# Kernel optimization log

Measured on AMD Instinct MI355X. Metric: run time of the kernel, lower is better.

Reference implementation:

```python
import jax, jax.numpy as jnp
import numpy as np

N_NODES = 500000   # embedding table / pi rows
K = 32             # mixture components (communities)
D = 64             # embedding dim
B = 65536          # batch of node ids


def setup_inputs() -> dict:
    key = jax.random.key(0)
    k1, k2, k3, k4, k5 = jax.random.split(key, 5)
    embedding = jax.random.normal(k1, (N_NODES, D), dtype=jnp.float32)
    centroid = jax.random.normal(k2, (K, D), dtype=jnp.float32)
    # SPD covariance per component: A A^T * s + I
    A = jax.random.normal(k3, (K, D, D), dtype=jnp.float32) * 0.1
    cov = jnp.einsum('kde,kfe->kdf', A, A) + jnp.eye(D, dtype=jnp.float32)[None]
    # responsibilities (rows sum to 1, like predict_proba output)
    pi = jax.nn.softmax(jax.random.normal(k4, (N_NODES, K), dtype=jnp.float32), axis=-1)
    input_labels = jax.random.randint(k5, (B,), 0, N_NODES)
    return {
        'embedding': embedding,
        'centroid': centroid,
        'cov': cov,
        'pi': pi,
        'input_labels': input_labels,
    }


def reference(embedding, centroid, cov, pi, input_labels):
    # x = node_embedding(input_labels): (B, D)
    x = embedding[input_labels]
    inv_cov = jnp.linalg.inv(cov)                 # (K, D, D)
    _, logdet = jnp.linalg.slogdet(cov)           # (K,)
    diff = x[:, None, :] - centroid[None, :, :]   # (B, K, D)
    # batched Mahalanobis distance per component: (B, K)
    quad = jnp.einsum('bkd,kde,bke->bk', diff, inv_cov, diff)
    log2pi = jnp.log(jnp.asarray(2.0 * np.pi, dtype=x.dtype))
    logpdf = -0.5 * (D * log2pi + logdet[None, :] + quad)  # (B, K)
    resp = pi[input_labels]                       # (B, K)
    # original: ret_loss = abs(sum_i sum_k pi[i,k] * logpdf[i,k])
    return jnp.abs(jnp.sum(resp * logpdf))
```

## Files before the change

kernel.cpp:

```cpp
#include <hip/hip_runtime.h>

#define LOG2PI 1.8378770664093453f
#define LN2    0.6931471805599453f

typedef short short8 __attribute__((ext_vector_type(8)));
typedef float f32x4 __attribute__((ext_vector_type(4)));

__device__ __forceinline__ unsigned short f2bf(float f) {
    unsigned int u = __builtin_bit_cast(unsigned int, f);
    u = (u + 0x7FFFu + ((u >> 16) & 1u)) >> 16;
    return (unsigned short)u;
}
__device__ __forceinline__ float bf2f(unsigned short h) {
    unsigned int u = ((unsigned int)h) << 16;
    return __builtin_bit_cast(float, u);
}
__device__ __forceinline__ short8 pack8(float4 f0, float4 f1) {
    short8 r;
    r[0] = (short)f2bf(f0.x); r[1] = (short)f2bf(f0.y);
    r[2] = (short)f2bf(f0.z); r[3] = (short)f2bf(f0.w);
    r[4] = (short)f2bf(f1.x); r[5] = (short)f2bf(f1.y);
    r[6] = (short)f2bf(f1.z); r[7] = (short)f2bf(f1.w);
    return r;
}
__device__ __forceinline__ float rdlane(float v, int lane) {
    return __builtin_bit_cast(float, __builtin_amdgcn_readlane(__builtin_bit_cast(int, v), lane));
}

__global__ __launch_bounds__(512) void prep_kernel(
    const float* __restrict__ cov, const float* __restrict__ centroid,
    unsigned short* __restrict__ wW, float* __restrict__ wV2,
    float* __restrict__ wC, float* __restrict__ wAcc)
{
    __shared__ float rowbuf[2][64];
    __shared__ float Mi[64 * 65];
    const int k = blockIdx.x;
    const int tid = threadIdx.x;
    const int w = tid >> 6;
    const int l = tid & 63;

    float a[8];
#pragma unroll
    for (int r = 0; r < 8; ++r)
        a[r] = cov[(size_t)k * 4096 + (w * 8 + r) * 64 + l];

    if (k == 0 && tid == 0) wAcc[0] = 0.0f;

    float ld2 = 0.0f;
    for (int phase = 0; phase < 8; ++phase) {
        const bool owner = (w == phase);
#pragma unroll
        for (int jr = 0; jr < 8; ++jr) {
            const int j = phase * 8 + jr;
            if (owner) rowbuf[jr & 1][l] = a[jr];
            __syncthreads();
            float prow = rowbuf[jr & 1][l];
            float p = rdlane(prow, j);
            float pinv = __builtin_amdgcn_rcpf(p);
            ld2 += __log2f(p);
            float rjs = prow * pinv;
            float rjsp = (l == j) ? 1.0f + pinv : rjs;
#pragma unroll
            for (int r = 0; r < 8; ++r) {
                float cji = rdlane(a[r], j);
                a[r] = fmaf(-cji, rjsp, a[r]);
            }
            if (owner) a[jr] = (l == j) ? pinv : rjs;
        }
    }

#pragma unroll
    for (int r = 0; r < 8; ++r) Mi[(w * 8 + r) * 65 + l] = a[r];
    __syncthreads();

    if (tid < 64) {
        const int t = tid;
        float cme = centroid[k * 64 + t];
        float y = 0.0f;
#pragma unroll
        for (int e = 0; e < 64; ++e)
            y = fmaf(Mi[t * 65 + e], rdlane(cme, e), y);
        wV2[k * 64 + t] = 2.0f * y;
        float cy = cme * y;
#pragma unroll
        for (int off = 32; off > 0; off >>= 1) cy += __shfl_down(cy, off);
        if (t == 0) wC[k] = 64.0f * LOG2PI + ld2 * LN2 + cy;
    }

    {
        const int m = l & 15, qd = l >> 4;
        const int ntl = tid >> 7, s2 = (tid >> 6) & 1;
        const int d = ntl * 16 + m;
        const int e0 = s2 * 32 + qd * 8;
        float4 f0, f1;
        f0.x = Mi[d * 65 + e0 + 0]; f0.y = Mi[d * 65 + e0 + 1];
        f0.z = Mi[d * 65 + e0 + 2]; f0.w = Mi[d * 65 + e0 + 3];
        f1.x = Mi[d * 65 + e0 + 4]; f1.y = Mi[d * 65 + e0 + 5];
        f1.z = Mi[d * 65 + e0 + 6]; f1.w = Mi[d * 65 + e0 + 7];
        short8 pk = pack8(f0, f1);
        ((uint4*)wW)[((k * 4 + ntl) * 2 + s2) * 64 + l] = __builtin_bit_cast(uint4, pk);
    }
}

__global__ __launch_bounds__(256) void main_kernel(
    const float* __restrict__ emb, const float* __restrict__ pi,
    const int* __restrict__ labels, const unsigned short* __restrict__ wW,
    const float* __restrict__ wV2, const float* __restrict__ wC,
    float* __restrict__ wAcc)
{
    __shared__ int lab[128];
    __shared__ unsigned short Xs[128 * 72];
    __shared__ float Rg[128 * 36];
    __shared__ float vq[2048];
    __shared__ float cdet[32];
    __shared__ float red[4];

    const int tid = threadIdx.x;
    const int row0 = blockIdx.x * 128;

    if (tid < 128) lab[tid] = labels[row0 + tid];
    if (tid < 32) cdet[tid] = wC[tid];
    {
        const float4* v4 = (const float4*)wV2;
        *(float4*)&vq[tid * 8]     = v4[tid * 2];
        *(float4*)&vq[tid * 8 + 4] = v4[tid * 2 + 1];
    }
    __syncthreads();

    {
        int r = tid >> 1, h = tid & 1;
        const float4* e4 = (const float4*)(emb + (size_t)lab[r] * 64 + h * 32);
#pragma unroll
        for (int q = 0; q < 4; ++q) {
            float4 f0 = e4[q * 2], f1 = e4[q * 2 + 1];
            short8 pk = pack8(f0, f1);
            *(short8*)&Xs[r * 72 + h * 32 + q * 8] = pk;
        }
    }
    {
        const float4* pi4 = (const float4*)pi;
#pragma unroll
        for (int it = 0; it < 4; ++it) {
            int id = it * 256 + tid;
            int r = id >> 3, c = id & 7;
            float4 f = pi4[(size_t)lab[r] * 8 + c];
            *(float4*)&Rg[r * 36 + c * 4] = f;
        }
    }
    __syncthreads();

    const int w = tid >> 6, l = tid & 63;
    const int m = l & 15, qd = l >> 4;

    short8 afr[8][2];
#pragma unroll
    for (int rt = 0; rt < 8; ++rt) {
        int row = rt * 16 + m;
#pragma unroll
        for (int s = 0; s < 2; ++s)
            afr[rt][s] = *(const short8*)&Xs[row * 72 + s * 32 + qd * 8];
    }

    float qa[8][4] = {};
    float part = 0.0f;
    const uint4* wf4 = (const uint4*)wW;

    for (int nt = 0; nt < 32; ++nt) {
        int gnt = w * 32 + nt;
        uint4 u0 = wf4[(gnt * 2 + 0) * 64 + l];
        uint4 u1 = wf4[(gnt * 2 + 1) * 64 + l];
        short8 b0 = __builtin_bit_cast(short8, u0);
        short8 b1 = __builtin_bit_cast(short8, u1);
        float vv = vq[gnt * 16 + m];
        int dcol = (nt & 3) * 16 + m;
#pragma unroll
        for (int rt = 0; rt < 8; ++rt) {
            f32x4 cc = {0.0f, 0.0f, 0.0f, 0.0f};
            cc = __builtin_amdgcn_mfma_f32_16x16x32_bf16(afr[rt][0], b0, cc, 0, 0, 0);
            cc = __builtin_amdgcn_mfma_f32_16x16x32_bf16(afr[rt][1], b1, cc, 0, 0, 0);
#pragma unroll
            for (int r2 = 0; r2 < 4; ++r2) {
                int rowl = rt * 16 + qd * 4 + r2;
                float xv = bf2f(Xs[rowl * 72 + dcol]);
                qa[rt][r2] = fmaf(xv, cc[r2] - vv, qa[rt][r2]);
            }
        }
        if ((nt & 3) == 3) {
            int kk = w * 8 + (nt >> 2);
            float cd = cdet[kk] * 0.0625f;
#pragma unroll
            for (int rt = 0; rt < 8; ++rt) {
#pragma unroll
                for (int r2 = 0; r2 < 4; ++r2) {
                    int rowl = rt * 16 + qd * 4 + r2;
                    part = fmaf(Rg[rowl * 36 + kk], qa[rt][r2] + cd, part);
                    qa[rt][r2] = 0.0f;
                }
            }
        }
    }

    for (int off = 32; off > 0; off >>= 1) part += __shfl_down(part, off);
    if (l == 0) red[w] = part;
    __syncthreads();
    if (tid == 0) atomicAdd(wAcc, red[0] + red[1] + red[2] + red[3]);
}

__global__ void fin_kernel(const float* __restrict__ wAcc, float* __restrict__ out) {
    out[0] = fabsf(0.5f * wAcc[0]);
}

extern "C" void kernel_launch(void* const* d_in, const int* in_sizes, int n_in,
                              void* d_out, int out_size, void* d_ws, size_t ws_size,
                              hipStream_t stream) {
    const float* emb    = (const float*)d_in[0];
    const float* cent   = (const float*)d_in[1];
    const float* cov    = (const float*)d_in[2];
    const float* pi     = (const float*)d_in[3];
    const int*   labels = (const int*)d_in[4];
    float* out = (float*)d_out;

    char* w = (char*)d_ws;
    unsigned short* wW = (unsigned short*)w;
    float* wV2 = (float*)(w + 262144);
    float* wC  = (float*)(w + 270336);
    float* wAcc = (float*)(w + 270464);

    prep_kernel<<<32, 512, 0, stream>>>(cov, cent, wW, wV2, wC, wAcc);
    main_kernel<<<512, 256, 0, stream>>>(emb, pi, labels, wW, wV2, wC, wAcc);
    fin_kernel<<<1, 1, 0, stream>>>(wAcc, out);
}
```

Measured before the change: 247.6 us.

## Permute bf16 K-dim layout to keep x values in registers, fuse final reduction

Permutes the bf16 packing order of embedding rows and inverse-covariance fragments so that each lane's x values for the Mahalanobis weighting land in two packed registers. These are loaded once instead of being read from LDS inside the MFMA loop. The component loop is restructured into explicit per-component blocks with the four column tiles unrolled. The separate finalize kernel is removed in favour of a last-block-done atomic counter, which saves a launch at the cost of more register pressure and extra atomics.

```diff
diff --git a/kernel.cpp b/kernel.cpp
--- a/kernel.cpp
+++ b/kernel.cpp
@@ -11,18 +11,6 @@
     u = (u + 0x7FFFu + ((u >> 16) & 1u)) >> 16;
     return (unsigned short)u;
 }
-__device__ __forceinline__ float bf2f(unsigned short h) {
-    unsigned int u = ((unsigned int)h) << 16;
-    return __builtin_bit_cast(float, u);
-}
-__device__ __forceinline__ short8 pack8(float4 f0, float4 f1) {
-    short8 r;
-    r[0] = (short)f2bf(f0.x); r[1] = (short)f2bf(f0.y);
-    r[2] = (short)f2bf(f0.z); r[3] = (short)f2bf(f0.w);
-    r[4] = (short)f2bf(f1.x); r[5] = (short)f2bf(f1.y);
-    r[6] = (short)f2bf(f1.z); r[7] = (short)f2bf(f1.w);
-    return r;
-}
 __device__ __forceinline__ float rdlane(float v, int lane) {
     return __builtin_bit_cast(float, __builtin_amdgcn_readlane(__builtin_bit_cast(int, v), lane));
 }
@@ -30,7 +18,7 @@
 __global__ __launch_bounds__(512) void prep_kernel(
     const float* __restrict__ cov, const float* __restrict__ centroid,
     unsigned short* __restrict__ wW, float* __restrict__ wV2,
-    float* __restrict__ wC, float* __restrict__ wAcc)
+    float* __restrict__ wC, float* __restrict__ wAcc, unsigned int* __restrict__ wCnt)
 {
     __shared__ float rowbuf[2][64];
     __shared__ float Mi[64 * 65];
@@ -44,7 +32,7 @@
     for (int r = 0; r < 8; ++r)
         a[r] = cov[(size_t)k * 4096 + (w * 8 + r) * 64 + l];
 
-    if (k == 0 && tid == 0) wAcc[0] = 0.0f;
+    if (k == 0 && tid == 0) { wAcc[0] = 0.0f; wCnt[0] = 0u; }
 
     float ld2 = 0.0f;
     for (int phase = 0; phase < 8; ++phase) {
@@ -91,13 +79,12 @@
         const int m = l & 15, qd = l >> 4;
         const int ntl = tid >> 7, s2 = (tid >> 6) & 1;
         const int d = ntl * 16 + m;
-        const int e0 = s2 * 32 + qd * 8;
-        float4 f0, f1;
-        f0.x = Mi[d * 65 + e0 + 0]; f0.y = Mi[d * 65 + e0 + 1];
-        f0.z = Mi[d * 65 + e0 + 2]; f0.w = Mi[d * 65 + e0 + 3];
-        f1.x = Mi[d * 65 + e0 + 4]; f1.y = Mi[d * 65 + e0 + 5];
-        f1.z = Mi[d * 65 + e0 + 6]; f1.w = Mi[d * 65 + e0 + 7];
-        short8 pk = pack8(f0, f1);
+        const int base = s2 * 8 + qd * 2;
+        const float* Mr = &Mi[d * 65];
+        short8 pk;
+#pragma unroll
+        for (int i = 0; i < 8; ++i)
+            pk[i] = (short)f2bf(Mr[(i & 3) * 16 + base + (i >> 2)]);
         ((uint4*)wW)[((k * 4 + ntl) * 2 + s2) * 64 + l] = __builtin_bit_cast(uint4, pk);
     }
 }
@@ -106,7 +93,8 @@
     const float* __restrict__ emb, const float* __restrict__ pi,
     const int* __restrict__ labels, const unsigned short* __restrict__ wW,
     const float* __restrict__ wV2, const float* __restrict__ wC,
-    float* __restrict__ wAcc)
+    float* __restrict__ wAcc, unsigned int* __restrict__ wCnt,
+    float* __restrict__ out)
 {
     __shared__ int lab[128];
     __shared__ unsigned short Xs[128 * 72];
@@ -129,12 +117,22 @@
 
     {
         int r = tid >> 1, h = tid & 1;
-        const float4* e4 = (const float4*)(emb + (size_t)lab[r] * 64 + h * 32);
-#pragma unroll
-        for (int q = 0; q < 4; ++q) {
-            float4 f0 = e4[q * 2], f1 = e4[q * 2 + 1];
-            short8 pk = pack8(f0, f1);
-            *(short8*)&Xs[r * 72 + h * 32 + q * 8] = pk;
+        const float* erow = emb + (size_t)lab[r] * 64 + h * 8;
+        float xv[4][8];
+#pragma unroll
+        for (int c16 = 0; c16 < 4; ++c16) {
+            float4 f0 = *(const float4*)(erow + c16 * 16);
+            float4 f1 = *(const float4*)(erow + c16 * 16 + 4);
+            xv[c16][0] = f0.x; xv[c16][1] = f0.y; xv[c16][2] = f0.z; xv[c16][3] = f0.w;
+            xv[c16][4] = f1.x; xv[c16][5] = f1.y; xv[c16][6] = f1.z; xv[c16][7] = f1.w;
+        }
+#pragma unroll
+        for (int g = 0; g < 4; ++g) {
+            short8 pk;
+#pragma unroll
+            for (int idx = 0; idx < 8; ++idx)
+                pk[idx] = (short)f2bf(xv[idx & 3][g * 2 + (idx >> 2)]);
+            *(short8*)&Xs[r * 72 + h * 32 + g * 8] = pk;
         }
     }
     {
@@ -160,54 +158,71 @@
         for (int s = 0; s < 2; ++s)
             afr[rt][s] = *(const short8*)&Xs[row * 72 + s * 32 + qd * 8];
     }
-
-    float qa[8][4] = {};
+    uint2 xr[8][4];
+#pragma unroll
+    for (int rt = 0; rt < 8; ++rt)
+#pragma unroll
+        for (int r2 = 0; r2 < 4; ++r2) {
+            int rowl = rt * 16 + qd * 4 + r2;
+            xr[rt][r2] = *(const uint2*)&Xs[rowl * 72 + m * 4];
+        }
+
     float part = 0.0f;
     const uint4* wf4 = (const uint4*)wW;
 
-    for (int nt = 0; nt < 32; ++nt) {
-        int gnt = w * 32 + nt;
-        uint4 u0 = wf4[(gnt * 2 + 0) * 64 + l];
-        uint4 u1 = wf4[(gnt * 2 + 1) * 64 + l];
-        short8 b0 = __builtin_bit_cast(short8, u0);
-        short8 b1 = __builtin_bit_cast(short8, u1);
-        float vv = vq[gnt * 16 + m];
-        int dcol = (nt & 3) * 16 + m;
-#pragma unroll
-        for (int rt = 0; rt < 8; ++rt) {
-            f32x4 cc = {0.0f, 0.0f, 0.0f, 0.0f};
-            cc = __builtin_amdgcn_mfma_f32_16x16x32_bf16(afr[rt][0], b0, cc, 0, 0, 0);
-            cc = __builtin_amdgcn_mfma_f32_16x16x32_bf16(afr[rt][1], b1, cc, 0, 0, 0);
+    for (int q = 0; q < 8; ++q) {
+        int kk = w * 8 + q;
+        float qa[8][4];
+#pragma unroll
+        for (int rt = 0; rt < 8; ++rt)
+#pragma unroll
+            for (int r2 = 0; r2 < 4; ++r2) qa[rt][r2] = 0.0f;
+
+#pragma unroll
+        for (int c16 = 0; c16 < 4; ++c16) {
+            int gnt = w * 32 + q * 4 + c16;
+            uint4 u0 = wf4[(gnt * 2 + 0) * 64 + l];
+            uint4 u1 = wf4[(gnt * 2 + 1) * 64 + l];
+            short8 b0 = __builtin_bit_cast(short8, u0);
+            short8 b1 = __builtin_bit_cast(short8, u1);
+            float vv = vq[gnt * 16 + m];
+#pragma unroll
+            for (int rt = 0; rt < 8; ++rt) {
+                f32x4 cc = {0.0f, 0.0f, 0.0f, 0.0f};
+                cc = __builtin_amdgcn_mfma_f32_16x16x32_bf16(afr[rt][0], b0, cc, 0, 0, 0);
+                cc = __builtin_amdgcn_mfma_f32_16x16x32_bf16(afr[rt][1], b1, cc, 0, 0, 0);
+#pragma unroll
+                for (int r2 = 0; r2 < 4; ++r2) {
+                    uint2 u = xr[rt][r2];
+                    unsigned int p = (c16 & 2) ? u.y : u.x;
+                    unsigned int bits = (c16 & 1) ? (p & 0xFFFF0000u) : (p << 16);
+                    float xvf = __builtin_bit_cast(float, bits);
+                    qa[rt][r2] = fmaf(xvf, cc[r2] - vv, qa[rt][r2]);
+                }
+            }
+        }
+        float cd = cdet[kk] * 0.0625f;
+#pragma unroll
+        for (int rt = 0; rt < 8; ++rt)
 #pragma unroll
             for (int r2 = 0; r2 < 4; ++r2) {
                 int rowl = rt * 16 + qd * 4 + r2;
-                float xv = bf2f(Xs[rowl * 72 + dcol]);
-                qa[rt][r2] = fmaf(xv, cc[r2] - vv, qa[rt][r2]);
+                part = fmaf(Rg[rowl * 36 + kk], qa[rt][r2] + cd, part);
             }
-        }
-        if ((nt & 3) == 3) {
-            int kk = w * 8 + (nt >> 2);
-            float cd = cdet[kk] * 0.0625f;
-#pragma unroll
-            for (int rt = 0; rt < 8; ++rt) {
-#pragma unroll
-                for (int r2 = 0; r2 < 4; ++r2) {
-                    int rowl = rt * 16 + qd * 4 + r2;
-                    part = fmaf(Rg[rowl * 36 + kk], qa[rt][r2] + cd, part);
-                    qa[rt][r2] = 0.0f;
-                }
-            }
-        }
     }
 
     for (int off = 32; off > 0; off >>= 1) part += __shfl_down(part, off);
     if (l == 0) red[w] = part;
     __syncthreads();
-    if (tid == 0) atomicAdd(wAcc, red[0] + red[1] + red[2] + red[3]);
-}
-
-__global__ void fin_kernel(const float* __restrict__ wAcc, float* __restrict__ out) {
-    out[0] = fabsf(0.5f * wAcc[0]);
+    if (tid == 0) {
+        atomicAdd(wAcc, red[0] + red[1] + red[2] + red[3]);
+        __threadfence();
+        unsigned int done = atomicAdd(wCnt, 1u);
+        if (done == gridDim.x - 1) {
+            float total = atomicAdd(wAcc, 0.0f);
+            out[0] = fabsf(0.5f * total);
+        }
+    }
 }
 
 extern "C" void kernel_launch(void* const* d_in, const int* in_sizes, int n_in,
@@ -225,8 +240,8 @@
     float* wV2 = (float*)(w + 262144);
     float* wC  = (float*)(w + 270336);
     float* wAcc = (float*)(w + 270464);
-
-    prep_kernel<<<32, 512, 0, stream>>>(cov, cent, wW, wV2, wC, wAcc);
-    main_kernel<<<512, 256, 0, stream>>>(emb, pi, labels, wW, wV2, wC, wAcc);
-    fin_kernel<<<1, 1, 0, stream>>>(wAcc, out);
-}
+    unsigned int* wCnt = (unsigned int*)(w + 270468);
+
+    prep_kernel<<<32, 512, 0, stream>>>(cov, cent, wW, wV2, wC, wAcc, wCnt);
+    main_kernel<<<512, 256, 0, stream>>>(emb, pi, labels, wW, wV2, wC, wAcc, wCnt, out);
+}
```

Measured after the change: 245.0 us. No clear change (-1.0%).
